# Performance work log

Measured on AMD Instinct MI355X. Metric: run time of the kernel, lower is better.

Reference implementation:

```python
import jax, jax.numpy as jnp
import numpy as np

B = 64        # graphs per batch
NP = 96       # nodes per graph
H = 64        # hid_size
IN_F = 32     # node feature dim
E_F = 16      # edge feature dim
DEG = 8       # avg degree
ENSEMBLE = 1


def _lin(key, fan_in, fan_out):
    return jax.random.normal(key, (fan_in, fan_out), jnp.float32) / np.float32(np.sqrt(fan_in))


def setup_inputs() -> dict:
    key = jax.random.key(0)
    ks = jax.random.split(key, 12)
    N = B * NP
    E = B * NP * DEG
    x = jax.random.normal(ks[0], (N, IN_F), jnp.float32)
    edge_attr = jax.random.normal(ks[1], (E, E_F), jnp.float32)
    # within-graph random edges (sorted per-graph blocks, like is_sorted=True)
    rng = np.random.default_rng(0)
    off = (np.arange(B) * NP)[:, None]
    src = (rng.integers(0, NP, size=(B, NP * DEG)) + off).ravel()
    dst = (rng.integers(0, NP, size=(B, NP * DEG)) + off).ravel()
    edge_index = jnp.asarray(np.stack([src, dst]), dtype=jnp.int32)
    # idx = concat of triu_indices(n, -n) per graph == ALL n^2 pairs per graph
    tri = np.triu_indices(NP, -NP)
    idx0 = jnp.asarray((tri[0][None, :] + off).ravel(), jnp.int32)  # [B*NP^2]
    idx1 = jnp.asarray((tri[1][None, :] + off).ravel(), jnp.int32)
    params = dict(
        W_atom=_lin(ks[2], IN_F, H), b_atom=jnp.zeros((H,), jnp.float32),
        W_bond=_lin(ks[3], E_F, H), b_bond=jnp.zeros((H,), jnp.float32),
        W_node=_lin(ks[4], H, H), b_node=jnp.zeros((H,), jnp.float32),
        W_edge=_lin(ks[5], H, H), b_edge=jnp.zeros((H,), jnp.float32),
        W1=_lin(ks[6], 3 * H, H), b1=jnp.zeros((H,), jnp.float32),
        W2=_lin(ks[7], H, H), b2=jnp.zeros((H,), jnp.float32),
        W3=_lin(ks[8], H, ENSEMBLE), b3=jnp.zeros((ENSEMBLE,), jnp.float32),
    )
    return dict(x=x, edge_attr=edge_attr, edge_index=edge_index,
                idx0=idx0, idx1=idx1, n=NP, **params)


def reference(x, edge_attr, edge_index, idx0, idx1, n,
              W_atom, b_atom, W_bond, b_bond, W_node, b_node,
              W_edge, b_edge, W1, b1, W2, b2, W3, b3):
    # encoders
    xh = x @ W_atom + b_atom                 # [N, H]
    eh = edge_attr @ W_bond + b_bond         # [E, H]
    emb_n = xh @ W_node + b_node             # [N, H]
    emb_e = eh @ W_edge + b_edge             # [E, H]
    # SparseTensor.to_dense() then gather at idx == scatter-add edge embeddings
    # into the per-graph dense pairwise slot (duplicates sum, missing = 0),
    # without materializing the O(N^2) adjacency.
    u, v = edge_index[0], edge_index[1]
    g = u // n
    pair_idx = g * (n * n) + (u - g * n) * n + (v - g * n)   # [E]
    P = idx0.shape[0]                         # B * n^2, idx enumerates all pairs row-major
    pair_e = jnp.zeros((P, emb_e.shape[1]), emb_e.dtype).at[pair_idx].add(emb_e)
    emb = jnp.concatenate((emb_n[idx0], emb_n[idx1], pair_e), axis=-1)  # [P, 3H]
    # MLP [3H, H, H, ensemble], plain last layer
    h = jax.nn.relu(emb @ W1 + b1)
    h = jax.nn.relu(h @ W2 + b2)
    return h @ W3 + b3                        # [P, ensemble]
```

## Files before the change

### kernel.cpp

```cpp
#include <hip/hip_runtime.h>

#define NPG 96
#define BGR 64
#define HID 64
#define INF 32
#define EF  16
#define DEG 8
#define NN  (BGR*NPG)
#define NE  (BGR*NPG*DEG)
#define EPG (NPG*DEG)
#define PPG (NPG*NPG)

typedef short bf16x8 __attribute__((ext_vector_type(8)));
typedef float f32x4  __attribute__((ext_vector_type(4)));

__device__ __forceinline__ unsigned rne2(float lo, float hi) {
    union { float f; unsigned u; } a, b; a.f = lo; b.f = hi;
    unsigned ua = a.u + 0x7FFF + ((a.u >> 16) & 1);
    unsigned ub = b.u + 0x7FFF + ((b.u >> 16) & 1);
    return (ua >> 16) | (ub & 0xFFFF0000u);
}
__device__ __forceinline__ unsigned short rne1(float x) {
    union { float f; unsigned u; } a; a.f = x;
    return (unsigned short)((a.u + 0x7FFF + ((a.u >> 16) & 1)) >> 16);
}

__global__ __launch_bounds__(256) void node_kernel(
    const float* __restrict__ x,
    const float* __restrict__ W_atom, const float* __restrict__ b_atom,
    const float* __restrict__ W_node, const float* __restrict__ b_node,
    const float* __restrict__ W1,     const float* __restrict__ b1,
    float* __restrict__ Abuf, float* __restrict__ Bbuf)
{
    __shared__ float sh[4][64];
    const int wave = threadIdx.x >> 6, lane = threadIdx.x & 63;
    const int n = __builtin_amdgcn_readfirstlane(blockIdx.x * 4 + wave);
    const float* xr = x + n * INF;

    float xh = b_atom[lane];
    #pragma unroll
    for (int k = 0; k < INF; ++k) xh += xr[k] * W_atom[k*HID + lane];
    sh[wave][lane] = xh;
    __syncthreads();

    float en = b_node[lane];
    #pragma unroll
    for (int k = 0; k < HID; ++k) en += sh[wave][k] * W_node[k*HID + lane];
    __syncthreads();
    sh[wave][lane] = en;
    __syncthreads();

    float a = b1[lane], b = 0.f;
    #pragma unroll
    for (int k = 0; k < HID; ++k) {
        const float ek = sh[wave][k];
        a += ek * W1[k*HID + lane];
        b += ek * W1[(HID + k)*HID + lane];
    }
    Abuf[n*HID + lane] = a;
    Bbuf[n*HID + lane] = b;
}

#define SBST 68
#define W2ST 72
__global__ __launch_bounds__(256) void pair_dense_kernel(
    const float* __restrict__ Abuf, const float* __restrict__ Bbuf,
    const float* __restrict__ W2,   const float* __restrict__ b2,
    const float* __restrict__ W3,   const float* __restrict__ b3,
    float* __restrict__ out)
{
    __shared__ float sB[NPG * SBST];
    __shared__ float sA[8 * 64];
    __shared__ unsigned short sW2t[64 * W2ST];
    const int t  = threadIdx.x;
    const int g  = blockIdx.x / 12;
    const int i0 = (blockIdx.x % 12) * 8;

    const float* Bg = Bbuf + g * NPG * 64;
    for (int idx = t; idx < NPG*64; idx += 256)
        sB[(idx >> 6)*SBST + (idx & 63)] = Bg[idx];
    for (int idx = t; idx < 8*64; idx += 256)
        sA[idx] = Abuf[(g*NPG + i0 + (idx >> 6))*64 + (idx & 63)];
    for (int idx = t; idx < 64*64; idx += 256) {
        const int k = idx >> 6, n = idx & 63;
        sW2t[n*W2ST + k] = rne1(W2[idx]);
    }
    __syncthreads();

    const int wave = t >> 6, lane = t & 63;
    const int col = lane & 15, q = lane >> 4;

    bf16x8 w2f[4][2];
    #pragma unroll
    for (int nt = 0; nt < 4; ++nt)
        #pragma unroll
        for (int c = 0; c < 2; ++c)
            w2f[nt][c] = *(const bf16x8*)(sW2t + (nt*16 + col)*W2ST + c*32 + q*8);

    float w3l[4], b2l[4];
    #pragma unroll
    for (int nt = 0; nt < 4; ++nt) {
        w3l[nt] = W3[nt*16 + col];
        b2l[nt] = b2[nt*16 + col];
    }
    const float b3v = b3[0];

    #pragma unroll
    for (int ii = 0; ii < 2; ++ii) {
        const int il = wave*2 + ii;
        float areg[16];
        {
            const float4* Ar = (const float4*)(sA + il*64 + q*8);
            const float4 a0 = Ar[0], a1 = Ar[1];
            const float4 a2 = Ar[8], a3 = Ar[9];
            areg[0]=a0.x; areg[1]=a0.y; areg[2]=a0.z; areg[3]=a0.w;
            areg[4]=a1.x; areg[5]=a1.y; areg[6]=a1.z; areg[7]=a1.w;
            areg[8]=a2.x; areg[9]=a2.y; areg[10]=a2.z; areg[11]=a2.w;
            areg[12]=a3.x; areg[13]=a3.y; areg[14]=a3.z; areg[15]=a3.w;
        }
        float* outr = out + g*PPG + (i0 + il)*NPG;

        for (int jc = 0; jc < 6; ++jc) {
            const int j0 = jc * 16;
            union { bf16x8 v; unsigned u[4]; } h1[2];
            const float* Brow = sB + (j0 + col)*SBST + q*8;
            #pragma unroll
            for (int c = 0; c < 2; ++c) {
                const float4 b0 = *(const float4*)(Brow + c*32);
                const float4 b1v = *(const float4*)(Brow + c*32 + 4);
                float h[8];
                h[0] = fmaxf(areg[c*8+0] + b0.x, 0.f);
                h[1] = fmaxf(areg[c*8+1] + b0.y, 0.f);
                h[2] = fmaxf(areg[c*8+2] + b0.z, 0.f);
                h[3] = fmaxf(areg[c*8+3] + b0.w, 0.f);
                h[4] = fmaxf(areg[c*8+4] + b1v.x, 0.f);
                h[5] = fmaxf(areg[c*8+5] + b1v.y, 0.f);
                h[6] = fmaxf(areg[c*8+6] + b1v.z, 0.f);
                h[7] = fmaxf(areg[c*8+7] + b1v.w, 0.f);
                #pragma unroll
                for (int p2 = 0; p2 < 4; ++p2)
                    h1[c].u[p2] = rne2(h[2*p2], h[2*p2+1]);
            }
            f32x4 acc[4];
            #pragma unroll
            for (int nt = 0; nt < 4; ++nt) {
                f32x4 z = {0.f, 0.f, 0.f, 0.f};
                z = __builtin_amdgcn_mfma_f32_16x16x32_bf16(h1[0].v, w2f[nt][0], z, 0, 0, 0);
                z = __builtin_amdgcn_mfma_f32_16x16x32_bf16(h1[1].v, w2f[nt][1], z, 0, 0, 0);
                acc[nt] = z;
            }
            float p[4];
            #pragma unroll
            for (int r = 0; r < 4; ++r) {
                float s = 0.f;
                #pragma unroll
                for (int nt = 0; nt < 4; ++nt)
                    s += fmaxf(acc[nt][r] + b2l[nt], 0.f) * w3l[nt];
                p[r] = s;
            }
            #pragma unroll
            for (int off = 1; off < 16; off <<= 1) {
                #pragma unroll
                for (int r = 0; r < 4; ++r)
                    p[r] += __shfl_xor(p[r], off, 64);
            }
            if (col == 0) {
                float4 o = make_float4(p[0]+b3v, p[1]+b3v, p[2]+b3v, p[3]+b3v);
                *(float4*)(outr + j0 + q*4) = o;
            }
        }
    }
}

__global__ __launch_bounds__(EPG) void dedup_kernel(
    const float* __restrict__ ea,  const int* __restrict__ eidx,
    int* __restrict__ fkey, int* __restrict__ fcnt,
    float* __restrict__ fsea, int* __restrict__ gcount)
{
    __shared__ int head[PPG];
    __shared__ int nxt[EPG];
    __shared__ int lcnt;
    const int t = threadIdx.x;
    const int g = blockIdx.x;

    for (int idx = t; idx < PPG; idx += EPG) head[idx] = -1;
    if (t == 0) lcnt = 0;

    const int u = eidx[g*EPG + t]      - g*NPG;
    const int v = eidx[NE + g*EPG + t] - g*NPG;
    const int key = u*NPG + v;
    __syncthreads();

    nxt[t] = atomicExch(&head[key], t);
    __syncthreads();

    if (head[key] == t) {
        const float* eag = ea + (size_t)g * EPG * EF;
        float s[EF];
        #pragma unroll
        for (int q = 0; q < EF; ++q) s[q] = 0.f;
        int cnt = 0;
        for (int e = t; e != -1; e = nxt[e]) {
            ++cnt;
            const float4* p = (const float4*)(eag + e*EF);
            #pragma unroll
            for (int q4 = 0; q4 < 4; ++q4) {
                const float4 f = p[q4];
                s[q4*4+0] += f.x; s[q4*4+1] += f.y;
                s[q4*4+2] += f.z; s[q4*4+3] += f.w;
            }
        }
        const int pos  = atomicAdd(&lcnt, 1);
        const int slot = g*EPG + pos;
        fkey[slot] = key;
        fcnt[slot] = cnt;
        #pragma unroll
        for (int q = 0; q < EF; ++q) fsea[slot*EF + q] = s[q];
    }
    __syncthreads();
    if (t == 0) gcount[g] = lcnt;
}

__global__ __launch_bounds__(256) void fixmlp_kernel(
    const float* __restrict__ Abuf, const float* __restrict__ Bbuf,
    const int* __restrict__ fkey, const int* __restrict__ fcnt,
    const float* __restrict__ fsea, const int* __restrict__ gcount,
    const float* __restrict__ W_bond, const float* __restrict__ b_bond,
    const float* __restrict__ W_edge, const float* __restrict__ b_edge,
    const float* __restrict__ W1,
    const float* __restrict__ W2,   const float* __restrict__ b2,
    const float* __restrict__ W3,   const float* __restrict__ b3,
    float* __restrict__ out)
{
    __shared__ float U[16*64];
    __shared__ float sWEc[16*64];
    __shared__ float sbc[64];
    const int t = threadIdx.x;

    for (int idx = t; idx < 16*64; idx += 256) {
        const int r = idx >> 6, c = idx & 63;
        float s = 0.f;
        for (int k = 0; k < 64; ++k) s += W_bond[r*64+k] * W_edge[k*64+c];
        U[idx] = s;
    }
    if (t < 64) {
        float s2 = b_edge[t];
        for (int k = 0; k < 64; ++k) s2 += b_bond[k] * W_edge[k*64+t];
        sbc[t] = s2;
    }
    __syncthreads();
    for (int idx = t; idx < 16*64; idx += 256) {
        const int r = idx >> 6, c = idx & 63;
        float s = 0.f;
        for (int k = 0; k < 64; ++k) s += U[r*64+k] * W1[(128+k)*64+c];
        sWEc[idx] = s;
    }
    __syncthreads();
    if (t < 64) {
        float sc = 0.f;
        for (int k = 0; k < 64; ++k) sc += sbc[k] * W1[(128+k)*64+t];
        __syncthreads();
        sbc[t] = sc;
    } else {
        __syncthreads();
    }
    __syncthreads();

    const int s = blockIdx.x * 256 + t;
    const int g = s / EPG;
    const int l = s % EPG;
    if (l >= gcount[g]) return;

    const int key = fkey[s];
    const float cntf = (float)fcnt[s];
    const int u = key / NPG, v = key % NPG;

    float se[EF];
    {
        const float4* p = (const float4*)(fsea + s*EF);
        #pragma unroll
        for (int q4 = 0; q4 < 4; ++q4) {
            const float4 f = p[q4];
            se[q4*4+0] = f.x; se[q4*4+1] = f.y;
            se[q4*4+2] = f.z; se[q4*4+3] = f.w;
        }
    }

    const float* Ar = Abuf + (g*NPG + u)*64;
    const float* Br = Bbuf + (g*NPG + v)*64;

    float h2[64];
    #pragma unroll
    for (int c = 0; c < 64; ++c) h2[c] = b2[c];

    for (int k = 0; k < 64; ++k) {
        float ck = cntf * sbc[k];
        #pragma unroll
        for (int q = 0; q < EF; ++q) ck += se[q] * sWEc[q*64 + k];
        float h1 = Ar[k] + Br[k] + ck;
        h1 = fmaxf(h1, 0.f);
        const float4* wrow = (const float4*)(W2 + k*64);
        #pragma unroll
        for (int c4 = 0; c4 < 16; ++c4) {
            const float4 w = wrow[c4];
            h2[c4*4+0] += h1 * w.x;
            h2[c4*4+1] += h1 * w.y;
            h2[c4*4+2] += h1 * w.z;
            h2[c4*4+3] += h1 * w.w;
        }
    }

    float acc = b3[0];
    #pragma unroll
    for (int c = 0; c < 64; ++c) acc += fmaxf(h2[c], 0.f) * W3[c];
    out[g*PPG + key] = acc;
}

extern "C" void kernel_launch(void* const* d_in, const int* in_sizes, int n_in,
                              void* d_out, int out_size, void* d_ws, size_t ws_size,
                              hipStream_t stream)
{
    const float* x      = (const float*)d_in[0];
    const float* ea     = (const float*)d_in[1];
    const int*   eidx   = (const int*)  d_in[2];
    const float* W_atom = (const float*)d_in[6];
    const float* b_atom = (const float*)d_in[7];
    const float* W_bond = (const float*)d_in[8];
    const float* b_bond = (const float*)d_in[9];
    const float* W_node = (const float*)d_in[10];
    const float* b_node = (const float*)d_in[11];
    const float* W_edge = (const float*)d_in[12];
    const float* b_edge = (const float*)d_in[13];
    const float* W1     = (const float*)d_in[14];
    const float* b1     = (const float*)d_in[15];
    const float* W2     = (const float*)d_in[16];
    const float* b2     = (const float*)d_in[17];
    const float* W3     = (const float*)d_in[18];
    const float* b3     = (const float*)d_in[19];
    float* out = (float*)d_out;

    float* ws    = (float*)d_ws;
    float* Abuf  = ws;
    float* Bbuf  = Abuf  + NN*HID;
    float* fsea  = Bbuf  + NN*HID;
    int*   fkey  = (int*)(fsea + NE*EF);
    int*   fcnt  = fkey + NE;
    int*   gcount= fcnt + NE;

    node_kernel<<<NN/4, 256, 0, stream>>>(x, W_atom, b_atom, W_node, b_node,
                                          W1, b1, Abuf, Bbuf);
    dedup_kernel<<<BGR, EPG, 0, stream>>>(ea, eidx, fkey, fcnt, fsea, gcount);
    pair_dense_kernel<<<BGR*12, 256, 0, stream>>>(Abuf, Bbuf,
                                                  W2, b2, W3, b3, out);
    fixmlp_kernel<<<NE/256, 256, 0, stream>>>(Abuf, Bbuf, fkey, fcnt, fsea,
                                              gcount, W_bond, b_bond,
                                              W_edge, b_edge, W1,
                                              W2, b2, W3, b3, out);
}
```

Measured before the change: 169.5 us.

## Precompute fused edge weights once and map fix-up slots to wavefronts

Block 0 of the dedup kernel now computes the folded edge-to-hidden weight matrix and bias once and writes them to workspace. Before, every fixmlp block recomputed them. The fixmlp kernel now gives each wavefront several deduplicated edge slots, with one hidden channel per lane. W2 is staged in shared memory, the second layer is done via shuffles, and the output is reduced across the wave. This removes the per-thread 64-float register accumulator and the redundant per-block weight folding, which should improve occupancy and coalescing. The cost is more blocks, cross-lane shuffle traffic, and serial weight precompute in one dedup block.

```diff
diff --git a/kernel.cpp b/kernel.cpp
--- a/kernel.cpp
+++ b/kernel.cpp
@@ -174,12 +174,18 @@
 
 __global__ __launch_bounds__(EPG) void dedup_kernel(
     const float* __restrict__ ea,  const int* __restrict__ eidx,
+    const float* __restrict__ W_bond, const float* __restrict__ b_bond,
+    const float* __restrict__ W_edge, const float* __restrict__ b_edge,
+    const float* __restrict__ W1,
     int* __restrict__ fkey, int* __restrict__ fcnt,
-    float* __restrict__ fsea, int* __restrict__ gcount)
-{
-    __shared__ int head[PPG];
-    __shared__ int nxt[EPG];
-    __shared__ int lcnt;
+    float* __restrict__ fsea, int* __restrict__ gcount,
+    float* __restrict__ wec, float* __restrict__ biascg)
+{
+    __shared__ int   head[PPG];
+    __shared__ int   nxt[EPG];
+    __shared__ float sU[16*64];
+    __shared__ float sbe[64];
+    __shared__ int   lcnt;
     const int t = threadIdx.x;
     const int g = blockIdx.x;
 
@@ -219,101 +225,91 @@
     }
     __syncthreads();
     if (t == 0) gcount[g] = lcnt;
-}
-
+
+    if (g == 0) {
+        for (int idx = t; idx < 16*64; idx += EPG) {
+            const int r = idx >> 6, c = idx & 63;
+            float s = 0.f;
+            for (int k = 0; k < 64; ++k) s += W_bond[r*64+k] * W_edge[k*64+c];
+            sU[idx] = s;
+        }
+        if (t < 64) {
+            float s2 = b_edge[t];
+            for (int k = 0; k < 64; ++k) s2 += b_bond[k] * W_edge[k*64+t];
+            sbe[t] = s2;
+        }
+        __syncthreads();
+        for (int idx = t; idx < 16*64; idx += EPG) {
+            const int r = idx >> 6, c = idx & 63;
+            float s = 0.f;
+            for (int k = 0; k < 64; ++k) s += sU[r*64+k] * W1[(128+k)*64+c];
+            wec[idx] = s;
+        }
+        if (t < 64) {
+            float sc = 0.f;
+            for (int k = 0; k < 64; ++k) sc += sbe[k] * W1[(128+k)*64+t];
+            biascg[t] = sc;
+        }
+    }
+}
+
+#define SLOTS_PER_WAVE 4
+#define FIX_BLOCKS ((BGR*EPG)/(4*SLOTS_PER_WAVE))
 __global__ __launch_bounds__(256) void fixmlp_kernel(
     const float* __restrict__ Abuf, const float* __restrict__ Bbuf,
     const int* __restrict__ fkey, const int* __restrict__ fcnt,
     const float* __restrict__ fsea, const int* __restrict__ gcount,
-    const float* __restrict__ W_bond, const float* __restrict__ b_bond,
-    const float* __restrict__ W_edge, const float* __restrict__ b_edge,
-    const float* __restrict__ W1,
+    const float* __restrict__ wec,  const float* __restrict__ biascg,
     const float* __restrict__ W2,   const float* __restrict__ b2,
     const float* __restrict__ W3,   const float* __restrict__ b3,
     float* __restrict__ out)
 {
-    __shared__ float U[16*64];
+    __shared__ float sW2[64*64];
     __shared__ float sWEc[16*64];
-    __shared__ float sbc[64];
+    __shared__ float sbc[64], sb2[64];
     const int t = threadIdx.x;
 
-    for (int idx = t; idx < 16*64; idx += 256) {
-        const int r = idx >> 6, c = idx & 63;
-        float s = 0.f;
-        for (int k = 0; k < 64; ++k) s += W_bond[r*64+k] * W_edge[k*64+c];
-        U[idx] = s;
-    }
-    if (t < 64) {
-        float s2 = b_edge[t];
-        for (int k = 0; k < 64; ++k) s2 += b_bond[k] * W_edge[k*64+t];
-        sbc[t] = s2;
-    }
-    __syncthreads();
-    for (int idx = t; idx < 16*64; idx += 256) {
-        const int r = idx >> 6, c = idx & 63;
-        float s = 0.f;
-        for (int k = 0; k < 64; ++k) s += U[r*64+k] * W1[(128+k)*64+c];
-        sWEc[idx] = s;
-    }
-    __syncthreads();
-    if (t < 64) {
-        float sc = 0.f;
-        for (int k = 0; k < 64; ++k) sc += sbc[k] * W1[(128+k)*64+t];
-        __syncthreads();
-        sbc[t] = sc;
-    } else {
-        __syncthreads();
-    }
-    __syncthreads();
-
-    const int s = blockIdx.x * 256 + t;
-    const int g = s / EPG;
-    const int l = s % EPG;
-    if (l >= gcount[g]) return;
-
-    const int key = fkey[s];
-    const float cntf = (float)fcnt[s];
-    const int u = key / NPG, v = key % NPG;
-
-    float se[EF];
-    {
-        const float4* p = (const float4*)(fsea + s*EF);
-        #pragma unroll
-        for (int q4 = 0; q4 < 4; ++q4) {
-            const float4 f = p[q4];
-            se[q4*4+0] = f.x; se[q4*4+1] = f.y;
-            se[q4*4+2] = f.z; se[q4*4+3] = f.w;
-        }
-    }
-
-    const float* Ar = Abuf + (g*NPG + u)*64;
-    const float* Br = Bbuf + (g*NPG + v)*64;
-
-    float h2[64];
-    #pragma unroll
-    for (int c = 0; c < 64; ++c) h2[c] = b2[c];
-
-    for (int k = 0; k < 64; ++k) {
-        float ck = cntf * sbc[k];
-        #pragma unroll
-        for (int q = 0; q < EF; ++q) ck += se[q] * sWEc[q*64 + k];
-        float h1 = Ar[k] + Br[k] + ck;
+    for (int idx = t; idx < 64*64; idx += 256) sW2[idx] = W2[idx];
+    for (int idx = t; idx < 16*64; idx += 256) sWEc[idx] = wec[idx];
+    if (t < 64) { sbc[t] = biascg[t]; sb2[t] = b2[t]; }
+    __syncthreads();
+
+    const int wave = t >> 6, lane = t & 63;
+    const int s0 = __builtin_amdgcn_readfirstlane(
+                       (blockIdx.x * 4 + wave) * SLOTS_PER_WAVE);
+    const float b3v = b3[0];
+    const float w3l = W3[lane];
+
+    #pragma unroll
+    for (int r = 0; r < SLOTS_PER_WAVE; ++r) {
+        const int s = s0 + r;
+        const int g = s / EPG;
+        const int l = s % EPG;
+        if (l >= gcount[g]) continue;
+
+        const int key = fkey[s];
+        const float cntf = (float)fcnt[s];
+        const int u = key / NPG, v = key % NPG;
+
+        float ck = cntf * sbc[lane];
+        const float* sep = fsea + (size_t)s * EF;
+        #pragma unroll
+        for (int q = 0; q < EF; ++q) ck += sep[q] * sWEc[q*64 + lane];
+
+        float h1 = Abuf[(g*NPG + u)*64 + lane] + Bbuf[(g*NPG + v)*64 + lane] + ck;
         h1 = fmaxf(h1, 0.f);
-        const float4* wrow = (const float4*)(W2 + k*64);
-        #pragma unroll
-        for (int c4 = 0; c4 < 16; ++c4) {
-            const float4 w = wrow[c4];
-            h2[c4*4+0] += h1 * w.x;
-            h2[c4*4+1] += h1 * w.y;
-            h2[c4*4+2] += h1 * w.z;
-            h2[c4*4+3] += h1 * w.w;
-        }
-    }
-
-    float acc = b3[0];
-    #pragma unroll
-    for (int c = 0; c < 64; ++c) acc += fmaxf(h2[c], 0.f) * W3[c];
-    out[g*PPG + key] = acc;
+
+        float h2 = sb2[lane];
+        #pragma unroll
+        for (int k = 0; k < 64; ++k)
+            h2 += __shfl(h1, k, 64) * sW2[k*64 + lane];
+
+        float p = fmaxf(h2, 0.f) * w3l;
+        #pragma unroll
+        for (int off = 32; off >= 1; off >>= 1)
+            p += __shfl_xor(p, off, 64);
+        if (lane == 0) out[g*PPG + key] = p + b3v;
+    }
 }
 
 extern "C" void kernel_launch(void* const* d_in, const int* in_sizes, int n_in,
@@ -346,14 +342,18 @@
     int*   fkey  = (int*)(fsea + NE*EF);
     int*   fcnt  = fkey + NE;
     int*   gcount= fcnt + NE;
+    float* wec   = (float*)(gcount + BGR);
+    float* biascg= wec + 16*64;
 
     node_kernel<<<NN/4, 256, 0, stream>>>(x, W_atom, b_atom, W_node, b_node,
                                           W1, b1, Abuf, Bbuf);
-    dedup_kernel<<<BGR, EPG, 0, stream>>>(ea, eidx, fkey, fcnt, fsea, gcount);
+    dedup_kernel<<<BGR, EPG, 0, stream>>>(ea, eidx, W_bond, b_bond,
+                                          W_edge, b_edge, W1,
+                                          fkey, fcnt, fsea, gcount,
+                                          wec, biascg);
     pair_dense_kernel<<<BGR*12, 256, 0, stream>>>(Abuf, Bbuf,
                                                   W2, b2, W3, b3, out);
-    fixmlp_kernel<<<NE/256, 256, 0, stream>>>(Abuf, Bbuf, fkey, fcnt, fsea,
-                                              gcount, W_bond, b_bond,
-                                              W_edge, b_edge, W1,
-                                              W2, b2, W3, b3, out);
-}
+    fixmlp_kernel<<<FIX_BLOCKS, 256, 0, stream>>>(
+        Abuf, Bbuf, fkey, fcnt, fsea, gcount, wec, biascg,
+        W2, b2, W3, b3, out);
+}
```

Result: slower. 193.6 us (+14.2%).
